# Kernel tuning notes

Measured on AMD Instinct MI355X. Metric: run time of the kernel, lower is better.

Reference implementation:

```python
import jax, jax.numpy as jnp
import numpy as np

MARGIN = 0.5
EPS = 1e-5


def setup_inputs() -> dict:
    key = jax.random.key(0)
    k1, k2 = jax.random.split(key)
    n, d, n_new, n_old = 8192, 256, 4096, 4096
    feature = jax.random.normal(k1, (n, d), dtype=jnp.float32)
    target = jax.random.randint(k2, (n,), 0, 100, dtype=jnp.int64)
    new_idx = jnp.arange(n_new, dtype=jnp.int64)
    old_idx = jnp.arange(n_old, dtype=jnp.int64)
    return {"feature": feature, "target": target, "new_idx": new_idx, "old_idx": old_idx}


def _triplet_loss(feature, target, new_idx, old_idx):
    n = feature.shape[0]
    n_new = new_idx.shape[0]
    # alpha switch is based on static shape, exactly as in the torch code
    alpha = 0.9 if old_idx.shape[0] != 0 else 0.5

    sim = feature @ feature.T                      # [n, n]
    sim_new = sim[:, new_idx]                      # [n, n_new]
    t_new = target[new_idx]                        # [n_new]

    same_new = target[:, None] == t_new[None, :]   # [n, n_new]
    is_new_row = jnp.arange(n) < n_new             # [n]

    # positive pairs (only defined for rows i < n_new)
    pos_mask = same_new & (sim_new < 1.0 - EPS)
    pos_loss_new = jnp.sum(jnp.where(pos_mask, 1.0 - sim_new, 0.0), axis=1)  # [n]
    # faithful to the torch bug: rows i >= n_new reuse the stale pos_pair_
    # from the last new row (i = n_new - 1)
    stale_pos = pos_loss_new[n_new - 1]
    pos_loss = jnp.where(is_new_row, pos_loss_new, stale_pos)

    # negatives: new rows scan all columns, old rows scan only new_idx columns
    diff_all = target[:, None] != target[None, :]
    neg_all = jnp.sum(jnp.where(diff_all & (sim > MARGIN), sim, 0.0), axis=1)
    neg_newcols = jnp.sum(jnp.where((~same_new) & (sim_new > MARGIN), sim_new, 0.0), axis=1)
    neg_loss = jnp.where(is_new_row, neg_all, neg_newcols)

    return jnp.mean(alpha * pos_loss + (1.0 - alpha) * neg_loss)


def reference(feature, target, new_idx, old_idx):
    return _triplet_loss(feature, target, new_idx, old_idx)
```

## Files before the change

kernel.cpp:

```cpp
#include <hip/hip_runtime.h>
#include <hip/hip_bf16.h>
#include <stdint.h>

#define MARGIN   0.5f
#define POS_THR  (1.0f - 1e-5f)

typedef __attribute__((ext_vector_type(8))) short  short8;
typedef __attribute__((ext_vector_type(4))) float  f32x4;

#define BM 128
#define BN 128
#define BK 32
#define NPANEL_SHIFT 7

__device__ __forceinline__ ushort f2bf_rne(float x) {
  uint32_t u = __float_as_uint(x);
  u += 0x7fffu + ((u >> 16) & 1u);
  return (ushort)(u >> 16);
}

__device__ __forceinline__ void async_load16(const ushort* g, ushort* l) {
  __builtin_amdgcn_global_load_lds(
      (__attribute__((address_space(1))) void*)(const_cast<ushort*>(g)),
      (__attribute__((address_space(3))) void*)(l),
      16, 0, 0);
}

__global__ void prep_kernel(const float* __restrict__ src, ushort* __restrict__ dst,
                            float* __restrict__ pos, float* __restrict__ neg,
                            int* __restrict__ cnt, int* __restrict__ flags,
                            int total4, int n, int npanel) {
  int i = blockIdx.x * blockDim.x + threadIdx.x;
  if (i < total4) {
    float4 v = reinterpret_cast<const float4*>(src)[i];
    ushort4 o;
    o.x = f2bf_rne(v.x); o.y = f2bf_rne(v.y);
    o.z = f2bf_rne(v.z); o.w = f2bf_rne(v.w);
    reinterpret_cast<ushort4*>(dst)[i] = o;
  }
  if (i < n) { pos[i] = 0.f; neg[i] = 0.f; cnt[i] = 0; }
  if (i < npanel) flags[i] = 0;
}

__global__ void count_kernel(const int* __restrict__ new_idx, int* __restrict__ cnt,
                             int* __restrict__ flags, int n_new) {
  int i = blockIdx.x * blockDim.x + threadIdx.x;
  if (i < n_new) {
    int idx = new_idx[i];
    atomicAdd(&cnt[idx], 1);
    atomicOr(&flags[idx >> NPANEL_SHIFT], 1);
  }
}

__global__ __launch_bounds__(256) void simloss_kernel(
    const ushort* __restrict__ fb, const int* __restrict__ target,
    const int* __restrict__ cnt, const int* __restrict__ colHasNew,
    float* __restrict__ pos_acc, float* __restrict__ neg_acc,
    int d, int n_new) {
  __shared__ __align__(16) ushort Als[2][BM * BK];
  __shared__ __align__(16) ushort Bls[2][BN * BK];
  __shared__ int   t_row[BM];
  __shared__ int   t_col[BN];
  __shared__ float cw_col[BN];

  const int tid = threadIdx.x;
  const int rowBase = blockIdx.y * BM;
  const int colBase = blockIdx.x * BN;

  if (rowBase >= n_new && colHasNew[blockIdx.x] == 0) return;

  if (tid < BM) t_row[tid] = target[rowBase + tid];
  if (tid < BN) {
    t_col[tid]  = target[colBase + tid];
    cw_col[tid] = (float)cnt[colBase + tid];
  }

  const int lane = tid & 63;
  const int wid  = tid >> 6;
  const int wr   = wid >> 1;
  const int wc   = wid & 1;
  const int l15  = lane & 15;
  const int kb   = lane >> 4;

  const int ch0 = (wid * 2 + 0) * 64 + lane;
  const int ch1 = (wid * 2 + 1) * 64 + lane;
  const int r0 = ch0 >> 2, kq0 = (ch0 & 3) ^ ((ch0 >> 3) & 3);
  const int r1 = ch1 >> 2, kq1 = (ch1 & 3) ^ ((ch1 >> 3) & 3);
  const ushort* gA0 = fb + (size_t)(rowBase + r0) * d + kq0 * 8;
  const ushort* gA1 = fb + (size_t)(rowBase + r1) * d + kq1 * 8;
  const ushort* gB0 = fb + (size_t)(colBase + r0) * d + kq0 * 8;
  const ushort* gB1 = fb + (size_t)(colBase + r1) * d + kq1 * 8;
  const int lo0 = (wid * 2 + 0) * 512;
  const int lo1 = (wid * 2 + 1) * 512;

  f32x4 acc[4][4] = {};

  int aoff[4], boff[4];
#pragma unroll
  for (int m = 0; m < 4; ++m) {
    int row = wr * 64 + m * 16 + l15;
    aoff[m] = row * 32 + ((kb ^ ((row >> 1) & 3)) * 8);
  }
#pragma unroll
  for (int nf = 0; nf < 4; ++nf) {
    int row = wc * 64 + nf * 16 + l15;
    boff[nf] = row * 32 + ((kb ^ ((row >> 1) & 3)) * 8);
  }

  async_load16(gA0, &Als[0][lo0]);
  async_load16(gA1, &Als[0][lo1]);
  async_load16(gB0, &Bls[0][lo0]);
  async_load16(gB1, &Bls[0][lo1]);
  __syncthreads();

  const int nk = d / BK;
  for (int t = 0; t < nk; ++t) {
    const int b = t & 1;
    if (t + 1 < nk) {
      int ko = (t + 1) * BK;
      async_load16(gA0 + ko, &Als[b ^ 1][lo0]);
      async_load16(gA1 + ko, &Als[b ^ 1][lo1]);
      async_load16(gB0 + ko, &Bls[b ^ 1][lo0]);
      async_load16(gB1 + ko, &Bls[b ^ 1][lo1]);
    }
    short8 afr[4], bfr[4];
#pragma unroll
    for (int m = 0; m < 4; ++m)
      afr[m] = *reinterpret_cast<const short8*>(&Als[b][aoff[m]]);
#pragma unroll
    for (int nf = 0; nf < 4; ++nf)
      bfr[nf] = *reinterpret_cast<const short8*>(&Bls[b][boff[nf]]);

#pragma unroll
    for (int m = 0; m < 4; ++m)
#pragma unroll
      for (int nf = 0; nf < 4; ++nf)
        acc[m][nf] = __builtin_amdgcn_mfma_f32_16x16x32_bf16(bfr[nf], afr[m], acc[m][nf], 0, 0, 0);
    __syncthreads();
  }

  int tc_r[4][4]; float cw_r[4][4];
#pragma unroll
  for (int nf = 0; nf < 4; ++nf)
#pragma unroll
    for (int q = 0; q < 4; ++q) {
      int cl = wc * 64 + nf * 16 + kb * 4 + q;
      tc_r[nf][q] = t_col[cl];
      cw_r[nf][q] = cw_col[cl];
    }

#pragma unroll
  for (int m = 0; m < 4; ++m) {
    int rl = wr * 64 + m * 16 + l15;
    int r  = rowBase + rl;
    int tr = t_row[rl];
    bool isnew = (r < n_new);
    float p = 0.f, ng = 0.f;
#pragma unroll
    for (int nf = 0; nf < 4; ++nf)
#pragma unroll
      for (int q = 0; q < 4; ++q) {
        float s = acc[m][nf][q];
        bool same = (tr == tc_r[nf][q]);
        if (isnew) {
          if (same && s < POS_THR)  p  += cw_r[nf][q] * (1.0f - s);
          if (!same && s > MARGIN)  ng += s;
        } else {
          if (!same && s > MARGIN)  ng += cw_r[nf][q] * s;
        }
      }
    p  += __shfl_xor(p, 16);  p  += __shfl_xor(p, 32);
    ng += __shfl_xor(ng, 16); ng += __shfl_xor(ng, 32);
    if (lane < 16) {
      if (p  != 0.f) atomicAdd(&pos_acc[r], p);
      if (ng != 0.f) atomicAdd(&neg_acc[r], ng);
    }
  }
}

__global__ void finalize_kernel(const float* __restrict__ pos_acc,
                                const float* __restrict__ neg_acc,
                                float* __restrict__ out, int n, int n_new,
                                float alpha) {
  float beta = 1.0f - alpha;
  float local = 0.f;
  int n4 = n >> 2;
  for (int i = threadIdx.x; i < n4; i += blockDim.x) {
    float4 pv = reinterpret_cast<const float4*>(pos_acc)[i];
    float4 nv = reinterpret_cast<const float4*>(neg_acc)[i];
    int r = i * 4;
    local += (r + 0 < n_new) ? alpha * pv.x + beta * nv.x : beta * nv.x;
    local += (r + 1 < n_new) ? alpha * pv.y + beta * nv.y : beta * nv.y;
    local += (r + 2 < n_new) ? alpha * pv.z + beta * nv.z : beta * nv.z;
    local += (r + 3 < n_new) ? alpha * pv.w + beta * nv.w : beta * nv.w;
  }
  if (threadIdx.x == 0 && n > n_new && n_new > 0)
    local += (float)(n - n_new) * alpha * pos_acc[n_new - 1];
#pragma unroll
  for (int off = 32; off; off >>= 1) local += __shfl_xor(local, off);
  __shared__ float red[4];
  int w = threadIdx.x >> 6, ln = threadIdx.x & 63;
  if (ln == 0) red[w] = local;
  __syncthreads();
  if (threadIdx.x == 0) out[0] = (red[0] + red[1] + red[2] + red[3]) / (float)n;
}

extern "C" void kernel_launch(void* const* d_in, const int* in_sizes, int n_in,
                              void* d_out, int out_size, void* d_ws, size_t ws_size,
                              hipStream_t stream) {
  const float* feature = (const float*)d_in[0];
  const int*   target  = (const int*)d_in[1];
  const int*   new_idx = (const int*)d_in[2];

  const int n     = in_sizes[1];
  const int d     = in_sizes[0] / n;
  const int n_new = in_sizes[2];
  const int n_old = (n_in > 3) ? in_sizes[3] : 0;
  const float alpha = (n_old != 0) ? 0.9f : 0.5f;
  const int npanel = n / BN;

  auto al = [](size_t x) { return (x + 255) & ~(size_t)255; };
  char* ws = (char*)d_ws;
  ushort* fb      = (ushort*)ws;
  size_t  off     = al((size_t)n * d * sizeof(ushort));
  float*  pos_acc = (float*)(ws + off); off += al((size_t)n * sizeof(float));
  float*  neg_acc = (float*)(ws + off); off += al((size_t)n * sizeof(float));
  int*    cnt     = (int*)(ws + off);   off += al((size_t)n * sizeof(int));
  int*    flags   = (int*)(ws + off);

  int total4 = (n * d) / 4;
  prep_kernel<<<(total4 + 255) / 256, 256, 0, stream>>>(feature, fb, pos_acc,
                                                        neg_acc, cnt, flags,
                                                        total4, n, npanel);
  count_kernel<<<(n_new + 255) / 256, 256, 0, stream>>>(new_idx, cnt, flags, n_new);

  dim3 grid(n / BN, n / BM);
  simloss_kernel<<<grid, 256, 0, stream>>>(fb, target, cnt, flags,
                                           pos_acc, neg_acc, d, n_new);

  finalize_kernel<<<1, 256, 0, stream>>>(pos_acc, neg_acc, (float*)d_out, n, n_new, alpha);
}
```

Before: 144.5 us.

## Triple-buffer GEMM K-loop with manual waitcnt and widen finalize block

Replaces the double-buffered LDS pipeline with a three-stage ring: two K-tiles are prefetched up front, and each iteration waits only for the oldest outstanding async loads (vmcnt) before one barrier, dropping the trailing __syncthreads. This is meant to hide more global-load latency and remove one barrier per K step. The cost is 50% more LDS per block, which may reduce occupancy, and explicit waitcnt/sched_barrier control that depends on exact load counts. The finalize kernel is also relaunched with 1024 threads and a generalized warp reduction.

```diff
diff --git a/kernel.cpp b/kernel.cpp
--- a/kernel.cpp
+++ b/kernel.cpp
@@ -57,8 +57,8 @@
     const int* __restrict__ cnt, const int* __restrict__ colHasNew,
     float* __restrict__ pos_acc, float* __restrict__ neg_acc,
     int d, int n_new) {
-  __shared__ __align__(16) ushort Als[2][BM * BK];
-  __shared__ __align__(16) ushort Bls[2][BN * BK];
+  __shared__ __align__(16) ushort Als[3][BM * BK];
+  __shared__ __align__(16) ushort Bls[3][BN * BK];
   __shared__ int   t_row[BM];
   __shared__ int   t_col[BN];
   __shared__ float cw_col[BN];
@@ -107,36 +107,54 @@
     boff[nf] = row * 32 + ((kb ^ ((row >> 1) & 3)) * 8);
   }
 
+  asm volatile("s_waitcnt vmcnt(0) lgkmcnt(0)" ::: "memory");
+  __builtin_amdgcn_sched_barrier(0);
+
   async_load16(gA0, &Als[0][lo0]);
   async_load16(gA1, &Als[0][lo1]);
   async_load16(gB0, &Bls[0][lo0]);
   async_load16(gB1, &Bls[0][lo1]);
-  __syncthreads();
-
   const int nk = d / BK;
+  if (nk > 1) {
+    async_load16(gA0 + BK, &Als[1][lo0]);
+    async_load16(gA1 + BK, &Als[1][lo1]);
+    async_load16(gB0 + BK, &Bls[1][lo0]);
+    async_load16(gB1 + BK, &Bls[1][lo1]);
+  }
+
+  int cur = 0;
   for (int t = 0; t < nk; ++t) {
-    const int b = t & 1;
-    if (t + 1 < nk) {
-      int ko = (t + 1) * BK;
-      async_load16(gA0 + ko, &Als[b ^ 1][lo0]);
-      async_load16(gA1 + ko, &Als[b ^ 1][lo1]);
-      async_load16(gB0 + ko, &Bls[b ^ 1][lo0]);
-      async_load16(gB1 + ko, &Bls[b ^ 1][lo1]);
+    if (t == nk - 1) asm volatile("s_waitcnt vmcnt(0)" ::: "memory");
+    else             asm volatile("s_waitcnt vmcnt(4)" ::: "memory");
+    __builtin_amdgcn_s_barrier();
+    __builtin_amdgcn_sched_barrier(0);
+
+    if (t + 2 < nk) {
+      int nxt = cur + 2; if (nxt >= 3) nxt -= 3;
+      int ko = (t + 2) * BK;
+      async_load16(gA0 + ko, &Als[nxt][lo0]);
+      async_load16(gA1 + ko, &Als[nxt][lo1]);
+      async_load16(gB0 + ko, &Bls[nxt][lo0]);
+      async_load16(gB1 + ko, &Bls[nxt][lo1]);
     }
+
     short8 afr[4], bfr[4];
 #pragma unroll
     for (int m = 0; m < 4; ++m)
-      afr[m] = *reinterpret_cast<const short8*>(&Als[b][aoff[m]]);
+      afr[m] = *reinterpret_cast<const short8*>(&Als[cur][aoff[m]]);
 #pragma unroll
     for (int nf = 0; nf < 4; ++nf)
-      bfr[nf] = *reinterpret_cast<const short8*>(&Bls[b][boff[nf]]);
+      bfr[nf] = *reinterpret_cast<const short8*>(&Bls[cur][boff[nf]]);
+    asm volatile("s_waitcnt lgkmcnt(0)" ::: "memory");
+    __builtin_amdgcn_sched_barrier(0);
 
 #pragma unroll
     for (int m = 0; m < 4; ++m)
 #pragma unroll
       for (int nf = 0; nf < 4; ++nf)
         acc[m][nf] = __builtin_amdgcn_mfma_f32_16x16x32_bf16(bfr[nf], afr[m], acc[m][nf], 0, 0, 0);
-    __syncthreads();
+
+    cur = (cur + 1 == 3) ? 0 : cur + 1;
   }
 
   int tc_r[4][4]; float cw_r[4][4];
@@ -178,10 +196,9 @@
   }
 }
 
-__global__ void finalize_kernel(const float* __restrict__ pos_acc,
-                                const float* __restrict__ neg_acc,
-                                float* __restrict__ out, int n, int n_new,
-                                float alpha) {
+__global__ __launch_bounds__(1024) void finalize_kernel(
+    const float* __restrict__ pos_acc, const float* __restrict__ neg_acc,
+    float* __restrict__ out, int n, int n_new, float alpha) {
   float beta = 1.0f - alpha;
   float local = 0.f;
   int n4 = n >> 2;
@@ -198,11 +215,16 @@
     local += (float)(n - n_new) * alpha * pos_acc[n_new - 1];
 #pragma unroll
   for (int off = 32; off; off >>= 1) local += __shfl_xor(local, off);
-  __shared__ float red[4];
+  __shared__ float red[16];
   int w = threadIdx.x >> 6, ln = threadIdx.x & 63;
   if (ln == 0) red[w] = local;
   __syncthreads();
-  if (threadIdx.x == 0) out[0] = (red[0] + red[1] + red[2] + red[3]) / (float)n;
+  if (threadIdx.x == 0) {
+    float s = 0.f;
+    int nw = blockDim.x >> 6;
+    for (int i = 0; i < nw; ++i) s += red[i];
+    out[0] = s / (float)n;
+  }
 }
 
 extern "C" void kernel_launch(void* const* d_in, const int* in_sizes, int n_in,
@@ -238,5 +260,5 @@
   simloss_kernel<<<grid, 256, 0, stream>>>(fb, target, cnt, flags,
                                            pos_acc, neg_acc, d, n_new);
 
-  finalize_kernel<<<1, 256, 0, stream>>>(pos_acc, neg_acc, (float*)d_out, n, n_new, alpha);
-}
+  finalize_kernel<<<1, 1024, 0, stream>>>(pos_acc, neg_acc, (float*)d_out, n, n_new, alpha);
+}
```

Result: no change. 142.0 us (-1.7%).
